# Performance work log

Measured on AMD Instinct MI355X. Metric: run time of the kernel, lower is better.

Reference implementation:

```python
import jax, jax.numpy as jnp
import numpy as np

D_MODEL = 1024
NUM_HEADS = 16
D_K = D_MODEL // NUM_HEADS
B, S = 4, 2048
NEG_INF = -1.0e9  # matches torch masked_fill value


def setup_inputs() -> dict:
    key = jax.random.key(0)
    ks = jax.random.split(key, 6)
    scale = 1.0 / np.sqrt(D_MODEL)
    x = jax.random.normal(ks[0], (B, S, D_MODEL), dtype=jnp.float32)
    # causal mask, broadcast over batch and heads: [1,1,S,S]
    mask = jnp.tril(jnp.ones((S, S), dtype=jnp.int32))[None, None]
    Wq = jax.random.normal(ks[1], (D_MODEL, D_MODEL), dtype=jnp.float32) * scale
    Wk = jax.random.normal(ks[2], (D_MODEL, D_MODEL), dtype=jnp.float32) * scale
    Wv = jax.random.normal(ks[3], (D_MODEL, D_MODEL), dtype=jnp.float32) * scale
    Wo = jax.random.normal(ks[4], (D_MODEL, D_MODEL), dtype=jnp.float32) * scale
    bq = jnp.zeros((D_MODEL,), jnp.float32)
    bk = jnp.zeros((D_MODEL,), jnp.float32)
    bv = jnp.zeros((D_MODEL,), jnp.float32)
    bo = jnp.zeros((D_MODEL,), jnp.float32)
    return {"x": x, "mask": mask, "Wq": Wq, "bq": bq, "Wk": Wk, "bk": bk,
            "Wv": Wv, "bv": bv, "Wo": Wo, "bo": bo}


def reference(x, mask, Wq, bq, Wk, bk, Wv, bv, Wo, bo):
    b, s, d = x.shape
    # projections (torch Linear: y = x @ W.T + b)
    q = (x @ Wq.T + bq).reshape(b, s, NUM_HEADS, D_K).transpose(0, 2, 1, 3)  # [B,H,S,Dk]
    k = (x @ Wk.T + bk).reshape(b, s, NUM_HEADS, D_K).transpose(0, 2, 1, 3)
    v = (x @ Wv.T + bv).reshape(b, s, NUM_HEADS, D_K).transpose(0, 2, 1, 3)
    scores = jnp.einsum("bhqd,bhkd->bhqk", q, k) / jnp.sqrt(jnp.float32(D_K))
    scores = jnp.where(mask == 0, NEG_INF, scores)
    attn = jax.nn.softmax(scores, axis=-1)
    out = jnp.einsum("bhqk,bhkd->bhqd", attn, v)  # [B,H,S,Dk]
    out = out.transpose(0, 2, 1, 3).reshape(b, s, d)
    return out @ Wo.T + bo
```

## Files before the change

### kernel.cpp

```cpp
#include <hip/hip_runtime.h>
#include <hip/hip_bf16.h>

#define D_MODEL 1024
#define NUM_HEADS 16
#define DK 64
#define BATCH 4
#define SEQ 2048

typedef __hip_bfloat16 bf16;
typedef __attribute__((ext_vector_type(8))) short bf16x8;
typedef __attribute__((ext_vector_type(4))) short bf16x4;
typedef __attribute__((ext_vector_type(4))) float f32x4;

typedef __attribute__((address_space(1))) const unsigned int gu32;
typedef __attribute__((address_space(3))) unsigned int lu32;

#define QSCALE (0.125f * 1.44269504089f)

__device__ __forceinline__ void gll16(const bf16* g, bf16* l) {
    __builtin_amdgcn_global_load_lds((gu32*)g, (lu32*)l, 16, 0, 0);
}

__global__ __launch_bounds__(256)
void cvt_bf16(const float* __restrict__ x,  const float* __restrict__ Wq,
              const float* __restrict__ Wk, const float* __restrict__ Wv,
              const float* __restrict__ Wo, bf16* __restrict__ xb,
              bf16* __restrict__ Wb)
{
    size_t v = (size_t)blockIdx.x * 256 + threadIdx.x;
    size_t e = v * 4;
    const float* src; bf16* dst; size_t off;
    if (e < 8388608) { src = x; dst = xb; off = e; }
    else {
        size_t r = e - 8388608;
        int w = (int)(r >> 20);
        off = r & 1048575;
        src = (w == 0) ? Wq : (w == 1) ? Wk : (w == 2) ? Wv : Wo;
        dst = Wb + ((size_t)w << 20);
    }
    float4 f = *(const float4*)(src + off);
    bf16 o[4] = {__float2bfloat16(f.x), __float2bfloat16(f.y),
                 __float2bfloat16(f.z), __float2bfloat16(f.w)};
    *(bf16x4*)(dst + off) = *(const bf16x4*)o;
}

__device__ __forceinline__ void stage_gll(const bf16* __restrict__ src,
                                          bf16* lds, int t, int k0)
{
    #pragma unroll
    for (int p = 0; p < 4; ++p) {
        int idx = t + p * 256;
        int row = idx >> 3, cl = idx & 7;
        int cg = cl ^ (row & 7);
        gll16(src + (size_t)row * 1024 + k0 + cg * 8, lds + idx * 8);
    }
}

__device__ __forceinline__ bf16x8 frag_ld(const bf16* lds, int row, int h, int quad) {
    return *(const bf16x8*)(lds + row * 64 + (((h << 2) + quad) ^ (row & 7)) * 8);
}

__global__ __launch_bounds__(256)
void gemm_qkv(const bf16* __restrict__ xb, const bf16* __restrict__ Wb,
              const float* __restrict__ bq, const float* __restrict__ bk,
              const float* __restrict__ bv,
              bf16* __restrict__ Q, bf16* __restrict__ Kt, bf16* __restrict__ Vtr)
{
    __shared__ bf16 As[128 * 64];
    __shared__ bf16 Bs[128 * 64];
    const int t = threadIdx.x;
    const int wave = t >> 6, lane = t & 63;
    const int quad = lane >> 4, l16 = lane & 15;
    const int wr = wave >> 1, wc = wave & 1;
    const int proj = blockIdx.x >> 3;
    const int colBase = (blockIdx.x & 7) * 128;
    const int rowBase = blockIdx.y * 128;

    const bf16* Ablk = xb + (size_t)rowBase * 1024;
    const bf16* Bblk = Wb + ((size_t)proj << 20) + (size_t)colBase * 1024;
    const float* bias = proj == 0 ? bq : (proj == 1 ? bk : bv);

    f32x4 acc[4][4];
    #pragma unroll
    for (int i = 0; i < 4; ++i)
        #pragma unroll
        for (int j = 0; j < 4; ++j) acc[i][j] = (f32x4){0.f, 0.f, 0.f, 0.f};

    for (int k0 = 0; k0 < 1024; k0 += 64) {
        stage_gll(Ablk, As, t, k0);
        stage_gll(Bblk, Bs, t, k0);
        __syncthreads();
        #pragma unroll
        for (int h = 0; h < 2; ++h) {
            bf16x8 af[4], bfr[4];
            #pragma unroll
            for (int i = 0; i < 4; ++i)
                af[i] = frag_ld(As, wr * 64 + i * 16 + l16, h, quad);
            #pragma unroll
            for (int j = 0; j < 4; ++j)
                bfr[j] = frag_ld(Bs, wc * 64 + j * 16 + l16, h, quad);
            #pragma unroll
            for (int i = 0; i < 4; ++i)
                #pragma unroll
                for (int j = 0; j < 4; ++j)
                    acc[i][j] = __builtin_amdgcn_mfma_f32_16x16x32_bf16(af[i], bfr[j],
                                                                        acc[i][j], 0, 0, 0);
        }
        __syncthreads();
    }

    float bias4[4];
    #pragma unroll
    for (int j = 0; j < 4; ++j)
        bias4[j] = bias[colBase + wc * 64 + j * 16 + l16];

    const float oscale = (proj == 0) ? QSCALE : 1.0f;

    #pragma unroll
    for (int i = 0; i < 4; ++i)
        #pragma unroll
        for (int rr = 0; rr < 4; ++rr) {
            int r = rowBase + wr * 64 + i * 16 + quad * 4 + rr;
            int b_ = r >> 11, s_ = r & 2047;
            #pragma unroll
            for (int j = 0; j < 4; ++j) {
                int c = colBase + wc * 64 + j * 16 + l16;
                float v = (acc[i][j][rr] + bias4[j]) * oscale;
                int h_ = c >> 6, d_ = c & 63;
                size_t bh = (size_t)(b_ * NUM_HEADS + h_);
                if (proj == 2)
                    Vtr[(bh * DK + d_) * SEQ + s_] = __float2bfloat16(v);
                else {
                    bf16* dst = proj == 0 ? Q : Kt;
                    dst[(bh * SEQ + s_) * DK + d_] = __float2bfloat16(v);
                }
            }
        }
}

__global__ __launch_bounds__(256)
void gemm_out(const bf16* __restrict__ ctx, const bf16* __restrict__ Wb,
              const float* __restrict__ bo, float* __restrict__ out)
{
    __shared__ bf16 As[128 * 64];
    __shared__ bf16 Bs[128 * 64];
    const int t = threadIdx.x;
    const int wave = t >> 6, lane = t & 63;
    const int quad = lane >> 4, l16 = lane & 15;
    const int wr = wave >> 1, wc = wave & 1;
    const int colBase = blockIdx.x * 128;
    const int rowBase = blockIdx.y * 128;

    const bf16* Ablk = ctx + (size_t)rowBase * 1024;
    const bf16* Bblk = Wb + ((size_t)3 << 20) + (size_t)colBase * 1024;

    f32x4 acc[4][4];
    #pragma unroll
    for (int i = 0; i < 4; ++i)
        #pragma unroll
        for (int j = 0; j < 4; ++j) acc[i][j] = (f32x4){0.f, 0.f, 0.f, 0.f};

    for (int k0 = 0; k0 < 1024; k0 += 64) {
        stage_gll(Ablk, As, t, k0);
        stage_gll(Bblk, Bs, t, k0);
        __syncthreads();
        #pragma unroll
        for (int h = 0; h < 2; ++h) {
            bf16x8 af[4], bfr[4];
            #pragma unroll
            for (int i = 0; i < 4; ++i)
                af[i] = frag_ld(As, wr * 64 + i * 16 + l16, h, quad);
            #pragma unroll
            for (int j = 0; j < 4; ++j)
                bfr[j] = frag_ld(Bs, wc * 64 + j * 16 + l16, h, quad);
            #pragma unroll
            for (int i = 0; i < 4; ++i)
                #pragma unroll
                for (int j = 0; j < 4; ++j)
                    acc[i][j] = __builtin_amdgcn_mfma_f32_16x16x32_bf16(af[i], bfr[j],
                                                                        acc[i][j], 0, 0, 0);
        }
        __syncthreads();
    }

    #pragma unroll
    for (int i = 0; i < 4; ++i)
        #pragma unroll
        for (int rr = 0; rr < 4; ++rr) {
            int r = rowBase + wr * 64 + i * 16 + quad * 4 + rr;
            #pragma unroll
            for (int j = 0; j < 4; ++j) {
                int c = colBase + wc * 64 + j * 16 + l16;
                out[(size_t)r * 1024 + c] = acc[i][j][rr] + bo[c];
            }
        }
}

#define AS 72

__device__ __forceinline__ void stage_attn(const bf16* __restrict__ Kb,
                                           const bf16* __restrict__ Vb,
                                           int k0, bf16* ks, bf16* vs, int t)
{
    #pragma unroll
    for (int p = 0; p < 2; ++p) {
        int idx = t + p * 256;
        int row = idx >> 3, cl = idx & 7;
        int cg = cl ^ (row & 7);
        gll16(Kb + (size_t)(k0 + row) * DK + cg * 8, ks + idx * 8);
        gll16(Vb + (size_t)row * SEQ + k0 + cg * 8, vs + idx * 8);
    }
}

__global__ __launch_bounds__(256)
void attn_mfma(const bf16* __restrict__ Q, const bf16* __restrict__ K,
               const bf16* __restrict__ Vt, bf16* __restrict__ ctx)
{
    __shared__ bf16 Ks[2][64 * 64];
    __shared__ bf16 Vs[2][64 * 64];
    __shared__ bf16 Ps[4][2][16 * AS];

    const int t    = threadIdx.x;
    const int wave = t >> 6, lane = t & 63;
    const int quad = lane >> 4, l16 = lane & 15;
    const int bh   = blockIdx.x;
    const int qbi  = 15 - blockIdx.y;
    const int b_ = bh >> 4, h_ = bh & 15;

    const bf16* Qb = Q  + (size_t)bh * SEQ * DK;
    const bf16* Kb = K  + (size_t)bh * SEQ * DK;
    const bf16* Vb = Vt + (size_t)bh * DK * SEQ;

    const int qb  = qbi * 128;
    const int ntiles = 2 * qbi + 2;

    bf16x8 qf[2][2];
    #pragma unroll
    for (int i = 0; i < 2; ++i) {
        const int qrow = qb + wave * 32 + i * 16 + l16;
        qf[i][0] = *(const bf16x8*)(Qb + (size_t)qrow * DK + quad * 8);
        qf[i][1] = *(const bf16x8*)(Qb + (size_t)qrow * DK + 32 + quad * 8);
    }

    f32x4 O[2][4];
    float lsum[2][4];
    #pragma unroll
    for (int i = 0; i < 2; ++i)
        #pragma unroll
        for (int nc = 0; nc < 4; ++nc) {
            O[i][nc] = (f32x4){0.f, 0.f, 0.f, 0.f};
            lsum[i][nc] = 0.f;
        }

    stage_attn(Kb, Vb, 0, Ks[0], Vs[0], t);
    __syncthreads();

    for (int kt = 0; kt < ntiles; ++kt) {
        const int cur = kt & 1;
        const int k0  = kt * 64;
        if (kt + 1 < ntiles)
            stage_attn(Kb, Vb, k0 + 64, Ks[cur ^ 1], Vs[cur ^ 1], t);

        const bool diag = (kt + 2 >= ntiles);
        const bool skip = (kt == ntiles - 1) && (wave < 2);

        if (!skip) {
            bf16x8 kf[4][2];
            #pragma unroll
            for (int h = 0; h < 4; ++h) {
                kf[h][0] = frag_ld(Ks[cur], h * 16 + l16, 0, quad);
                kf[h][1] = frag_ld(Ks[cur], h * 16 + l16, 1, quad);
            }

            #pragma unroll
            for (int i = 0; i < 2; ++i) {
                const int qrow0i = qb + wave * 32 + i * 16;
                float lacc[4];
                #pragma unroll
                for (int r = 0; r < 4; ++r) lacc[r] = lsum[i][r];
                #pragma unroll
                for (int h = 0; h < 4; ++h) {
                    f32x4 a = (f32x4){0.f, 0.f, 0.f, 0.f};
                    a = __builtin_amdgcn_mfma_f32_16x16x32_bf16(qf[i][0], kf[h][0], a, 0, 0, 0);
                    a = __builtin_amdgcn_mfma_f32_16x16x32_bf16(qf[i][1], kf[h][1], a, 0, 0, 0);
                    #pragma unroll
                    for (int r = 0; r < 4; ++r) {
                        float ss = a[r];
                        if (diag && (k0 + h * 16 + l16 > qrow0i + quad * 4 + r))
                            ss = -1e30f;
                        float p = exp2f(ss);
                        lacc[r] += p;
                        Ps[wave][i][(quad * 4 + r) * AS + h * 16 + l16] =
                            __float2bfloat16(p);
                    }
                }
                #pragma unroll
                for (int r = 0; r < 4; ++r) lsum[i][r] = lacc[r];
            }

            bf16x8 pf[2][2];
            #pragma unroll
            for (int i = 0; i < 2; ++i) {
                pf[i][0] = *(const bf16x8*)(&Ps[wave][i][l16 * AS + quad * 8]);
                pf[i][1] = *(const bf16x8*)(&Ps[wave][i][l16 * AS + 32 + quad * 8]);
            }
            __builtin_amdgcn_s_setprio(1);
            #pragma unroll
            for (int nc = 0; nc < 4; ++nc) {
                bf16x8 vf0 = frag_ld(Vs[cur], nc * 16 + l16, 0, quad);
                bf16x8 vf1 = frag_ld(Vs[cur], nc * 16 + l16, 1, quad);
                #pragma unroll
                for (int i = 0; i < 2; ++i) {
                    O[i][nc] = __builtin_amdgcn_mfma_f32_16x16x32_bf16(pf[i][0], vf0, O[i][nc], 0, 0, 0);
                    O[i][nc] = __builtin_amdgcn_mfma_f32_16x16x32_bf16(pf[i][1], vf1, O[i][nc], 0, 0, 0);
                }
            }
            __builtin_amdgcn_s_setprio(0);
        }
        __syncthreads();
    }

    #pragma unroll
    for (int i = 0; i < 2; ++i) {
        #pragma unroll
        for (int r = 0; r < 4; ++r) {
            #pragma unroll
            for (int off = 1; off < 16; off <<= 1)
                lsum[i][r] += __shfl_xor(lsum[i][r], off, 64);
        }
        #pragma unroll
        for (int nc = 0; nc < 4; ++nc)
            #pragma unroll
            for (int r = 0; r < 4; ++r) {
                const int row = qb + wave * 32 + i * 16 + quad * 4 + r;
                float v = O[i][nc][r] / lsum[i][r];
                ctx[((size_t)(b_ * SEQ + row)) * D_MODEL + h_ * DK + nc * 16 + l16] =
                    __float2bfloat16(v);
            }
    }
}

extern "C" void kernel_launch(void* const* d_in, const int* in_sizes, int n_in,
                              void* d_out, int out_size, void* d_ws, size_t ws_size,
                              hipStream_t stream) {
    const float* x  = (const float*)d_in[0];
    const float* Wq = (const float*)d_in[2];
    const float* bq = (const float*)d_in[3];
    const float* Wk = (const float*)d_in[4];
    const float* bk = (const float*)d_in[5];
    const float* Wv = (const float*)d_in[6];
    const float* bv = (const float*)d_in[7];
    const float* Wo = (const float*)d_in[8];
    const float* bo = (const float*)d_in[9];
    float* out = (float*)d_out;

    const size_t per = (size_t)BATCH * NUM_HEADS * SEQ * DK;
    bf16* Q   = (bf16*)d_ws;
    bf16* Kt  = Q  + per;
    bf16* Vtr = Kt + per;
    bf16* xb  = Vtr + per;
    bf16* ctx = xb;
    bf16* Wb  = xb + per;

    hipLaunchKernelGGL(cvt_bf16, dim3(12288), dim3(256), 0, stream,
                       x, Wq, Wk, Wv, Wo, xb, Wb);

    hipLaunchKernelGGL(gemm_qkv, dim3(24, 64), dim3(256), 0, stream,
                       xb, Wb, bq, bk, bv, Q, Kt, Vtr);

    hipLaunchKernelGGL(attn_mfma, dim3(64, 16), dim3(256), 0,
                       stream, Q, Kt, Vtr, ctx);

    hipLaunchKernelGGL(gemm_out, dim3(8, 64), dim3(256), 0, stream, ctx, Wb, bo, out);
}
```

Measured before the change: 304.8 us.

## Replace QKV and output GEMMs with 256x256 double-buffered pipelined kernel

Merges the QKV and output projection GEMMs into one templated kernel using 256x256 block tiles, 512 threads, and a two-stage LDS double buffer. The buffer is filled via global_load_lds two k-steps ahead, with explicit vmcnt waits and barriers. MFMA sections get raised wave priority. This aims to hide global load latency and raise data reuse per tile. In exchange, the much larger tiles shrink the grid (only 128 blocks for the output projection), which may leave CUs idle. The 128KB of LDS per block likely allows only one block per CU.

```diff
diff --git a/kernel.cpp b/kernel.cpp
--- a/kernel.cpp
+++ b/kernel.cpp
@@ -19,6 +19,10 @@
 
 __device__ __forceinline__ void gll16(const bf16* g, bf16* l) {
     __builtin_amdgcn_global_load_lds((gu32*)g, (lu32*)l, 16, 0, 0);
+}
+
+__device__ __forceinline__ bf16x8 frag_ld(const bf16* lds, int row, int h, int quad) {
+    return *(const bf16x8*)(lds + row * 64 + (((h << 2) + quad) ^ (row & 7)) * 8);
 }
 
 __global__ __launch_bounds__(256)
@@ -44,156 +48,144 @@
     *(bf16x4*)(dst + off) = *(const bf16x4*)o;
 }
 
-__device__ __forceinline__ void stage_gll(const bf16* __restrict__ src,
-                                          bf16* lds, int t, int k0)
+template<int MODE>
+__global__ __launch_bounds__(512, 2)
+void gemm_pipe(const bf16* __restrict__ A, const bf16* __restrict__ W,
+               const float* __restrict__ bqv, const float* __restrict__ bkv,
+               const float* __restrict__ bvv,
+               bf16* __restrict__ Q, bf16* __restrict__ Kt, bf16* __restrict__ Vtr,
+               float* __restrict__ fout)
 {
-    #pragma unroll
-    for (int p = 0; p < 4; ++p) {
-        int idx = t + p * 256;
-        int row = idx >> 3, cl = idx & 7;
-        int cg = cl ^ (row & 7);
-        gll16(src + (size_t)row * 1024 + k0 + cg * 8, lds + idx * 8);
-    }
-}
-
-__device__ __forceinline__ bf16x8 frag_ld(const bf16* lds, int row, int h, int quad) {
-    return *(const bf16x8*)(lds + row * 64 + (((h << 2) + quad) ^ (row & 7)) * 8);
-}
-
-__global__ __launch_bounds__(256)
-void gemm_qkv(const bf16* __restrict__ xb, const bf16* __restrict__ Wb,
-              const float* __restrict__ bq, const float* __restrict__ bk,
-              const float* __restrict__ bv,
-              bf16* __restrict__ Q, bf16* __restrict__ Kt, bf16* __restrict__ Vtr)
-{
-    __shared__ bf16 As[128 * 64];
-    __shared__ bf16 Bs[128 * 64];
+    __shared__ bf16 lds[65536];
+
     const int t = threadIdx.x;
     const int wave = t >> 6, lane = t & 63;
     const int quad = lane >> 4, l16 = lane & 15;
-    const int wr = wave >> 1, wc = wave & 1;
-    const int proj = blockIdx.x >> 3;
-    const int colBase = (blockIdx.x & 7) * 128;
-    const int rowBase = blockIdx.y * 128;
-
-    const bf16* Ablk = xb + (size_t)rowBase * 1024;
-    const bf16* Bblk = Wb + ((size_t)proj << 20) + (size_t)colBase * 1024;
-    const float* bias = proj == 0 ? bq : (proj == 1 ? bk : bv);
-
-    f32x4 acc[4][4];
-    #pragma unroll
-    for (int i = 0; i < 4; ++i)
-        #pragma unroll
-        for (int j = 0; j < 4; ++j) acc[i][j] = (f32x4){0.f, 0.f, 0.f, 0.f};
-
-    for (int k0 = 0; k0 < 1024; k0 += 64) {
-        stage_gll(Ablk, As, t, k0);
-        stage_gll(Bblk, Bs, t, k0);
-        __syncthreads();
-        #pragma unroll
-        for (int h = 0; h < 2; ++h) {
-            bf16x8 af[4], bfr[4];
-            #pragma unroll
-            for (int i = 0; i < 4; ++i)
-                af[i] = frag_ld(As, wr * 64 + i * 16 + l16, h, quad);
-            #pragma unroll
-            for (int j = 0; j < 4; ++j)
-                bfr[j] = frag_ld(Bs, wc * 64 + j * 16 + l16, h, quad);
-            #pragma unroll
-            for (int i = 0; i < 4; ++i)
-                #pragma unroll
-                for (int j = 0; j < 4; ++j)
-                    acc[i][j] = __builtin_amdgcn_mfma_f32_16x16x32_bf16(af[i], bfr[j],
-                                                                        acc[i][j], 0, 0, 0);
-        }
-        __syncthreads();
-    }
-
-    float bias4[4];
-    #pragma unroll
-    for (int j = 0; j < 4; ++j)
-        bias4[j] = bias[colBase + wc * 64 + j * 16 + l16];
-
-    const float oscale = (proj == 0) ? QSCALE : 1.0f;
-
-    #pragma unroll
-    for (int i = 0; i < 4; ++i)
-        #pragma unroll
-        for (int rr = 0; rr < 4; ++rr) {
-            int r = rowBase + wr * 64 + i * 16 + quad * 4 + rr;
-            int b_ = r >> 11, s_ = r & 2047;
-            #pragma unroll
-            for (int j = 0; j < 4; ++j) {
-                int c = colBase + wc * 64 + j * 16 + l16;
-                float v = (acc[i][j][rr] + bias4[j]) * oscale;
-                int h_ = c >> 6, d_ = c & 63;
-                size_t bh = (size_t)(b_ * NUM_HEADS + h_);
-                if (proj == 2)
-                    Vtr[(bh * DK + d_) * SEQ + s_] = __float2bfloat16(v);
-                else {
-                    bf16* dst = proj == 0 ? Q : Kt;
-                    dst[(bh * SEQ + s_) * DK + d_] = __float2bfloat16(v);
+    const int wm = wave >> 2, wn = wave & 3;
+
+    int proj, colb;
+    if (MODE == 0) { proj = blockIdx.x >> 2; colb = blockIdx.x & 3; }
+    else           { proj = 3;               colb = blockIdx.x;     }
+    const int rowBase = blockIdx.y * 256;
+
+    const bf16* Ablk = A + (size_t)rowBase * 1024;
+    const bf16* Bblk = W + ((size_t)proj << 20) + (size_t)colb * 256 * 1024;
+
+    auto stage_tile = [&](int d, int k0) {
+        bf16* Ad = lds + d * 16384;
+        bf16* Bd = lds + 32768 + d * 16384;
+        #pragma unroll
+        for (int h = 0; h < 2; ++h)
+            #pragma unroll
+            for (int p = 0; p < 2; ++p) {
+                int idx = t + p * 512;
+                int row = idx >> 3, cl = idx & 7, cg = cl ^ (row & 7);
+                gll16(Ablk + (size_t)(h * 128 + row) * 1024 + k0 + cg * 8,
+                      Ad + h * 8192 + idx * 8);
+                gll16(Bblk + (size_t)(h * 128 + row) * 1024 + k0 + cg * 8,
+                      Bd + h * 8192 + idx * 8);
+            }
+    };
+
+    f32x4 acc[8][4];
+    #pragma unroll
+    for (int mf = 0; mf < 8; ++mf)
+        #pragma unroll
+        for (int nf = 0; nf < 4; ++nf) acc[mf][nf] = (f32x4){0.f, 0.f, 0.f, 0.f};
+
+    auto compute_tile = [&](int d) {
+        const bf16* As = lds + d * 16384 + wm * 8192;
+        const bf16* Bs = lds + 32768 + d * 16384 + (wn >> 1) * 8192;
+        const int brow = (wn & 1) * 64;
+        bf16x8 bfr[4][2];
+        #pragma unroll
+        for (int nf = 0; nf < 4; ++nf) {
+            bfr[nf][0] = frag_ld(Bs, brow + nf * 16 + l16, 0, quad);
+            bfr[nf][1] = frag_ld(Bs, brow + nf * 16 + l16, 1, quad);
+        }
+        __builtin_amdgcn_s_setprio(1);
+        #pragma unroll
+        for (int mf = 0; mf < 8; ++mf) {
+            bf16x8 af0 = frag_ld(As, mf * 16 + l16, 0, quad);
+            bf16x8 af1 = frag_ld(As, mf * 16 + l16, 1, quad);
+            #pragma unroll
+            for (int nf = 0; nf < 4; ++nf) {
+                acc[mf][nf] = __builtin_amdgcn_mfma_f32_16x16x32_bf16(af0, bfr[nf][0], acc[mf][nf], 0, 0, 0);
+                acc[mf][nf] = __builtin_amdgcn_mfma_f32_16x16x32_bf16(af1, bfr[nf][1], acc[mf][nf], 0, 0, 0);
+            }
+        }
+        __builtin_amdgcn_s_setprio(0);
+    };
+
+    stage_tile(0, 0);
+    stage_tile(1, 64);
+    asm volatile("s_waitcnt vmcnt(8)" ::: "memory");
+    __builtin_amdgcn_s_barrier();
+    asm volatile("" ::: "memory");
+    __builtin_amdgcn_sched_barrier(0);
+
+    for (int kt = 0; kt < 16; ++kt) {
+        const int d = kt & 1;
+        compute_tile(d);
+
+        asm volatile("s_waitcnt lgkmcnt(0)" ::: "memory");
+        __builtin_amdgcn_sched_barrier(0);
+        __builtin_amdgcn_s_barrier();
+        asm volatile("" ::: "memory");
+
+        if (kt + 2 < 16) {
+            stage_tile(d, (kt + 2) * 64);
+            asm volatile("s_waitcnt vmcnt(8)" ::: "memory");
+        } else if (kt + 1 < 16) {
+            asm volatile("s_waitcnt vmcnt(0)" ::: "memory");
+        }
+        if (kt + 1 < 16) {
+            __builtin_amdgcn_s_barrier();
+            asm volatile("" ::: "memory");
+            __builtin_amdgcn_sched_barrier(0);
+        }
+    }
+
+    if (MODE == 0) {
+        const float* bias = proj == 0 ? bqv : (proj == 1 ? bkv : bvv);
+        float bias4[4];
+        #pragma unroll
+        for (int nf = 0; nf < 4; ++nf)
+            bias4[nf] = bias[colb * 256 + wn * 64 + nf * 16 + l16];
+        const float oscale = proj == 0 ? QSCALE : 1.0f;
+        #pragma unroll
+        for (int mf = 0; mf < 8; ++mf)
+            #pragma unroll
+            for (int rr = 0; rr < 4; ++rr) {
+                int r = rowBase + wm * 128 + mf * 16 + quad * 4 + rr;
+                int b_ = r >> 11, s_ = r & 2047;
+                #pragma unroll
+                for (int nf = 0; nf < 4; ++nf) {
+                    int c = colb * 256 + wn * 64 + nf * 16 + l16;
+                    float v = (acc[mf][nf][rr] + bias4[nf]) * oscale;
+                    int h_ = c >> 6, d_ = c & 63;
+                    size_t bh = (size_t)(b_ * NUM_HEADS + h_);
+                    if (proj == 2)
+                        Vtr[(bh * DK + d_) * SEQ + s_] = __float2bfloat16(v);
+                    else {
+                        bf16* dst = proj == 0 ? Q : Kt;
+                        dst[(bh * SEQ + s_) * DK + d_] = __float2bfloat16(v);
+                    }
                 }
             }
-        }
-}
-
-__global__ __launch_bounds__(256)
-void gemm_out(const bf16* __restrict__ ctx, const bf16* __restrict__ Wb,
-              const float* __restrict__ bo, float* __restrict__ out)
-{
-    __shared__ bf16 As[128 * 64];
-    __shared__ bf16 Bs[128 * 64];
-    const int t = threadIdx.x;
-    const int wave = t >> 6, lane = t & 63;
-    const int quad = lane >> 4, l16 = lane & 15;
-    const int wr = wave >> 1, wc = wave & 1;
-    const int colBase = blockIdx.x * 128;
-    const int rowBase = blockIdx.y * 128;
-
-    const bf16* Ablk = ctx + (size_t)rowBase * 1024;
-    const bf16* Bblk = Wb + ((size_t)3 << 20) + (size_t)colBase * 1024;
-
-    f32x4 acc[4][4];
-    #pragma unroll
-    for (int i = 0; i < 4; ++i)
-        #pragma unroll
-        for (int j = 0; j < 4; ++j) acc[i][j] = (f32x4){0.f, 0.f, 0.f, 0.f};
-
-    for (int k0 = 0; k0 < 1024; k0 += 64) {
-        stage_gll(Ablk, As, t, k0);
-        stage_gll(Bblk, Bs, t, k0);
-        __syncthreads();
-        #pragma unroll
-        for (int h = 0; h < 2; ++h) {
-            bf16x8 af[4], bfr[4];
-            #pragma unroll
-            for (int i = 0; i < 4; ++i)
-                af[i] = frag_ld(As, wr * 64 + i * 16 + l16, h, quad);
-            #pragma unroll
-            for (int j = 0; j < 4; ++j)
-                bfr[j] = frag_ld(Bs, wc * 64 + j * 16 + l16, h, quad);
-            #pragma unroll
-            for (int i = 0; i < 4; ++i)
-                #pragma unroll
-                for (int j = 0; j < 4; ++j)
-                    acc[i][j] = __builtin_amdgcn_mfma_f32_16x16x32_bf16(af[i], bfr[j],
-                                                                        acc[i][j], 0, 0, 0);
-        }
-        __syncthreads();
-    }
-
-    #pragma unroll
-    for (int i = 0; i < 4; ++i)
-        #pragma unroll
-        for (int rr = 0; rr < 4; ++rr) {
-            int r = rowBase + wr * 64 + i * 16 + quad * 4 + rr;
-            #pragma unroll
-            for (int j = 0; j < 4; ++j) {
-                int c = colBase + wc * 64 + j * 16 + l16;
-                out[(size_t)r * 1024 + c] = acc[i][j][rr] + bo[c];
-            }
-        }
+    } else {
+        #pragma unroll
+        for (int mf = 0; mf < 8; ++mf)
+            #pragma unroll
+            for (int rr = 0; rr < 4; ++rr) {
+                int r = rowBase + wm * 128 + mf * 16 + quad * 4 + rr;
+                #pragma unroll
+                for (int nf = 0; nf < 4; ++nf) {
+                    int c = colb * 256 + wn * 64 + nf * 16 + l16;
+                    fout[(size_t)r * 1024 + c] = acc[mf][nf][rr] + bqv[c];
+                }
+            }
+    }
 }
 
 #define AS 72
@@ -365,11 +357,13 @@
     hipLaunchKernelGGL(cvt_bf16, dim3(12288), dim3(256), 0, stream,
                        x, Wq, Wk, Wv, Wo, xb, Wb);
 
-    hipLaunchKernelGGL(gemm_qkv, dim3(24, 64), dim3(256), 0, stream,
-                       xb, Wb, bq, bk, bv, Q, Kt, Vtr);
+    hipLaunchKernelGGL((gemm_pipe<0>), dim3(12, 32), dim3(512), 0, stream,
+                       xb, Wb, bq, bk, bv, Q, Kt, Vtr, (float*)nullptr);
 
     hipLaunchKernelGGL(attn_mfma, dim3(64, 16), dim3(256), 0,
                        stream, Q, Kt, Vtr, ctx);
 
-    hipLaunchKernelGGL(gemm_out, dim3(8, 64), dim3(256), 0, stream, ctx, Wb, bo, out);
-}
+    hipLaunchKernelGGL((gemm_pipe<1>), dim3(4, 32), dim3(512), 0, stream,
+                       ctx, Wb, bo, (const float*)nullptr, (const float*)nullptr,
+                       (bf16*)nullptr, (bf16*)nullptr, (bf16*)nullptr, out);
+}
```

After: 312.3 us. 2.5% more time.

## Rewrite QKV GEMM with 256x256 tiles and double-buffered LDS staging

Applied to the files above, without the earlier changes.

The QKV projection GEMM moves from 128x128 tiles with 256 threads and single-buffered K=64 staging to 256x256 tiles with 512 threads. It uses a double-buffered K=32 LDS pipeline that issues the next tile's global-to-LDS loads before the current MFMAs, plus setprio around the MFMA block. This aims to raise arithmetic intensity and overlap loads with compute, at the cost of more accumulator registers and a grid of only 384 blocks. The change also hoists the output bias into registers and replaces the per-element divide in attention normalization with a reciprocal-multiply.

```diff
diff --git a/kernel.cpp b/kernel.cpp
--- a/kernel.cpp
+++ b/kernel.cpp
@@ -19,6 +19,14 @@
 
 __device__ __forceinline__ void gll16(const bf16* g, bf16* l) {
     __builtin_amdgcn_global_load_lds((gu32*)g, (lu32*)l, 16, 0, 0);
+}
+
+__device__ __forceinline__ bf16x8 frag_ld(const bf16* lds, int row, int h, int quad) {
+    return *(const bf16x8*)(lds + row * 64 + (((h << 2) + quad) ^ (row & 7)) * 8);
+}
+
+__device__ __forceinline__ bf16x8 frag_ld32(const bf16* lds, int row, int quad) {
+    return *(const bf16x8*)(lds + row * 32 + ((quad ^ (row & 3))) * 8);
 }
 
 __global__ __launch_bounds__(256)
@@ -44,8 +52,105 @@
     *(bf16x4*)(dst + off) = *(const bf16x4*)o;
 }
 
-__device__ __forceinline__ void stage_gll(const bf16* __restrict__ src,
-                                          bf16* lds, int t, int k0)
+__global__ __launch_bounds__(512, 4)
+void gemm_qkv(const bf16* __restrict__ A, const bf16* __restrict__ W,
+              const float* __restrict__ bqv, const float* __restrict__ bkv,
+              const float* __restrict__ bvv,
+              bf16* __restrict__ Q, bf16* __restrict__ Kt, bf16* __restrict__ Vtr)
+{
+    __shared__ bf16 lds[32768];
+
+    const int t = threadIdx.x;
+    const int wave = t >> 6, lane = t & 63;
+    const int quad = lane >> 4, l16 = lane & 15;
+    const int wm = wave >> 2, wn = wave & 3;
+
+    const int colb = blockIdx.x;
+    const int rowBase = blockIdx.y * 256;
+
+    const bf16* Ablk = A + (size_t)rowBase * 1024;
+    const bf16* Bblk = W + (size_t)colb * 256 * 1024;
+
+    auto stage = [&](int d, int k0) {
+        bf16* buf = (bf16*)lds + d * 16384;
+        #pragma unroll
+        for (int p = 0; p < 2; ++p) {
+            int idx = t + p * 512;
+            int row = idx >> 2, cg = (idx & 3) ^ (row & 3);
+            gll16(Ablk + (size_t)row * 1024 + k0 + cg * 8, buf + idx * 8);
+            gll16(Bblk + (size_t)row * 1024 + k0 + cg * 8, buf + 8192 + idx * 8);
+        }
+    };
+
+    f32x4 acc[8][4];
+    #pragma unroll
+    for (int mf = 0; mf < 8; ++mf)
+        #pragma unroll
+        for (int nf = 0; nf < 4; ++nf) acc[mf][nf] = (f32x4){0.f, 0.f, 0.f, 0.f};
+
+    stage(0, 0);
+    __syncthreads();
+
+    for (int kt = 0; kt < 32; ++kt) {
+        const int cur = kt & 1;
+        if (kt + 1 < 32) stage(cur ^ 1, (kt + 1) * 32);
+
+        const bf16* As = (const bf16*)lds + cur * 16384;
+        const bf16* Bs = As + 8192;
+
+        bf16x8 bfr[4];
+        #pragma unroll
+        for (int nf = 0; nf < 4; ++nf)
+            bfr[nf] = frag_ld32(Bs, wn * 64 + nf * 16 + l16, quad);
+
+        __builtin_amdgcn_s_setprio(1);
+        #pragma unroll
+        for (int mf = 0; mf < 8; ++mf) {
+            bf16x8 af = frag_ld32(As, wm * 128 + mf * 16 + l16, quad);
+            #pragma unroll
+            for (int nf = 0; nf < 4; ++nf)
+                acc[mf][nf] = __builtin_amdgcn_mfma_f32_16x16x32_bf16(
+                    af, bfr[nf], acc[mf][nf], 0, 0, 0);
+        }
+        __builtin_amdgcn_s_setprio(0);
+
+        __syncthreads();
+    }
+
+    {
+        const int proj = colb >> 2;
+        const float* bias = proj == 0 ? bqv : (proj == 1 ? bkv : bvv);
+        const int cb = (colb & 3) * 256;
+        float bias4[4];
+        #pragma unroll
+        for (int nf = 0; nf < 4; ++nf)
+            bias4[nf] = bias[cb + wn * 64 + nf * 16 + l16];
+        const float oscale = proj == 0 ? QSCALE : 1.0f;
+        #pragma unroll
+        for (int mf = 0; mf < 8; ++mf)
+            #pragma unroll
+            for (int rr = 0; rr < 4; ++rr) {
+                int r = rowBase + wm * 128 + mf * 16 + quad * 4 + rr;
+                int b_ = r >> 11, s_ = r & 2047;
+                #pragma unroll
+                for (int nf = 0; nf < 4; ++nf) {
+                    int c = cb + wn * 64 + nf * 16 + l16;
+                    float v = (acc[mf][nf][rr] + bias4[nf]) * oscale;
+                    int h_ = c >> 6, d_ = c & 63;
+                    size_t bh = (size_t)(b_ * NUM_HEADS + h_);
+                    if (proj == 2)
+                        Vtr[(bh * DK + d_) * SEQ + s_] = __float2bfloat16(v);
+                    else {
+                        bf16* dst = proj == 0 ? Q : Kt;
+                        dst[(bh * SEQ + s_) * DK + d_] = __float2bfloat16(v);
+                    }
+                }
+            }
+    }
+}
+
+__device__ __forceinline__ void stage_gll128(const bf16* __restrict__ src,
+                                             bf16* lds, int t, int k0)
 {
     #pragma unroll
     for (int p = 0; p < 4; ++p) {
@@ -54,88 +159,6 @@
         int cg = cl ^ (row & 7);
         gll16(src + (size_t)row * 1024 + k0 + cg * 8, lds + idx * 8);
     }
-}
-
-__device__ __forceinline__ bf16x8 frag_ld(const bf16* lds, int row, int h, int quad) {
-    return *(const bf16x8*)(lds + row * 64 + (((h << 2) + quad) ^ (row & 7)) * 8);
-}
-
-__global__ __launch_bounds__(256)
-void gemm_qkv(const bf16* __restrict__ xb, const bf16* __restrict__ Wb,
-              const float* __restrict__ bq, const float* __restrict__ bk,
-              const float* __restrict__ bv,
-              bf16* __restrict__ Q, bf16* __restrict__ Kt, bf16* __restrict__ Vtr)
-{
-    __shared__ bf16 As[128 * 64];
-    __shared__ bf16 Bs[128 * 64];
-    const int t = threadIdx.x;
-    const int wave = t >> 6, lane = t & 63;
-    const int quad = lane >> 4, l16 = lane & 15;
-    const int wr = wave >> 1, wc = wave & 1;
-    const int proj = blockIdx.x >> 3;
-    const int colBase = (blockIdx.x & 7) * 128;
-    const int rowBase = blockIdx.y * 128;
-
-    const bf16* Ablk = xb + (size_t)rowBase * 1024;
-    const bf16* Bblk = Wb + ((size_t)proj << 20) + (size_t)colBase * 1024;
-    const float* bias = proj == 0 ? bq : (proj == 1 ? bk : bv);
-
-    f32x4 acc[4][4];
-    #pragma unroll
-    for (int i = 0; i < 4; ++i)
-        #pragma unroll
-        for (int j = 0; j < 4; ++j) acc[i][j] = (f32x4){0.f, 0.f, 0.f, 0.f};
-
-    for (int k0 = 0; k0 < 1024; k0 += 64) {
-        stage_gll(Ablk, As, t, k0);
-        stage_gll(Bblk, Bs, t, k0);
-        __syncthreads();
-        #pragma unroll
-        for (int h = 0; h < 2; ++h) {
-            bf16x8 af[4], bfr[4];
-            #pragma unroll
-            for (int i = 0; i < 4; ++i)
-                af[i] = frag_ld(As, wr * 64 + i * 16 + l16, h, quad);
-            #pragma unroll
-            for (int j = 0; j < 4; ++j)
-                bfr[j] = frag_ld(Bs, wc * 64 + j * 16 + l16, h, quad);
-            #pragma unroll
-            for (int i = 0; i < 4; ++i)
-                #pragma unroll
-                for (int j = 0; j < 4; ++j)
-                    acc[i][j] = __builtin_amdgcn_mfma_f32_16x16x32_bf16(af[i], bfr[j],
-                                                                        acc[i][j], 0, 0, 0);
-        }
-        __syncthreads();
-    }
-
-    float bias4[4];
-    #pragma unroll
-    for (int j = 0; j < 4; ++j)
-        bias4[j] = bias[colBase + wc * 64 + j * 16 + l16];
-
-    const float oscale = (proj == 0) ? QSCALE : 1.0f;
-
-    #pragma unroll
-    for (int i = 0; i < 4; ++i)
-        #pragma unroll
-        for (int rr = 0; rr < 4; ++rr) {
-            int r = rowBase + wr * 64 + i * 16 + quad * 4 + rr;
-            int b_ = r >> 11, s_ = r & 2047;
-            #pragma unroll
-            for (int j = 0; j < 4; ++j) {
-                int c = colBase + wc * 64 + j * 16 + l16;
-                float v = (acc[i][j][rr] + bias4[j]) * oscale;
-                int h_ = c >> 6, d_ = c & 63;
-                size_t bh = (size_t)(b_ * NUM_HEADS + h_);
-                if (proj == 2)
-                    Vtr[(bh * DK + d_) * SEQ + s_] = __float2bfloat16(v);
-                else {
-                    bf16* dst = proj == 0 ? Q : Kt;
-                    dst[(bh * SEQ + s_) * DK + d_] = __float2bfloat16(v);
-                }
-            }
-        }
 }
 
 __global__ __launch_bounds__(256)
@@ -161,8 +184,8 @@
         for (int j = 0; j < 4; ++j) acc[i][j] = (f32x4){0.f, 0.f, 0.f, 0.f};
 
     for (int k0 = 0; k0 < 1024; k0 += 64) {
-        stage_gll(Ablk, As, t, k0);
-        stage_gll(Bblk, Bs, t, k0);
+        stage_gll128(Ablk, As, t, k0);
+        stage_gll128(Bblk, Bs, t, k0);
         __syncthreads();
         #pragma unroll
         for (int h = 0; h < 2; ++h) {
@@ -183,6 +206,11 @@
         __syncthreads();
     }
 
+    float bias4[4];
+    #pragma unroll
+    for (int j = 0; j < 4; ++j)
+        bias4[j] = bo[colBase + wc * 64 + j * 16 + l16];
+
     #pragma unroll
     for (int i = 0; i < 4; ++i)
         #pragma unroll
@@ -191,7 +219,7 @@
             #pragma unroll
             for (int j = 0; j < 4; ++j) {
                 int c = colBase + wc * 64 + j * 16 + l16;
-                out[(size_t)r * 1024 + c] = acc[i][j][rr] + bo[c];
+                out[(size_t)r * 1024 + c] = acc[i][j][rr] + bias4[j];
             }
         }
 }
@@ -322,18 +350,20 @@
 
     #pragma unroll
     for (int i = 0; i < 2; ++i) {
+        float inv[4];
         #pragma unroll
         for (int r = 0; r < 4; ++r) {
             #pragma unroll
             for (int off = 1; off < 16; off <<= 1)
                 lsum[i][r] += __shfl_xor(lsum[i][r], off, 64);
+            inv[r] = __builtin_amdgcn_rcpf(lsum[i][r]);
         }
         #pragma unroll
         for (int nc = 0; nc < 4; ++nc)
             #pragma unroll
             for (int r = 0; r < 4; ++r) {
                 const int row = qb + wave * 32 + i * 16 + quad * 4 + r;
-                float v = O[i][nc][r] / lsum[i][r];
+                float v = O[i][nc][r] * inv[r];
                 ctx[((size_t)(b_ * SEQ + row)) * D_MODEL + h_ * DK + nc * 16 + l16] =
                     __float2bfloat16(v);
             }
@@ -365,11 +395,12 @@
     hipLaunchKernelGGL(cvt_bf16, dim3(12288), dim3(256), 0, stream,
                        x, Wq, Wk, Wv, Wo, xb, Wb);
 
-    hipLaunchKernelGGL(gemm_qkv, dim3(24, 64), dim3(256), 0, stream,
+    hipLaunchKernelGGL(gemm_qkv, dim3(12, 32), dim3(512), 0, stream,
                        xb, Wb, bq, bk, bv, Q, Kt, Vtr);
 
     hipLaunchKernelGGL(attn_mfma, dim3(64, 16), dim3(256), 0,
                        stream, Q, Kt, Vtr, ctx);
 
-    hipLaunchKernelGGL(gemm_out, dim3(8, 64), dim3(256), 0, stream, ctx, Wb, bo, out);
-}
+    hipLaunchKernelGGL(gemm_out, dim3(8, 64), dim3(256), 0, stream,
+                       ctx, Wb, bo, out);
+}
```

After: 551.7 us. 81.0% more time.
